# Kernel optimization log

Measured on AMD Instinct MI355X. Metric: run time of the kernel, lower is better.

## Reference

```python
import jax, jax.numpy as jnp
import numpy as np

IN_FEATURES = 4096
OUT_FEATURES = 4096
B, S = 4, 2048


def setup_inputs() -> dict:
    key = jax.random.key(0)
    k_x, k_w, k_ws, k_ss, k_b = jax.random.split(key, 5)
    x = jax.random.normal(k_x, (B, S, IN_FEATURES), dtype=jnp.float32)
    weight_quantized = jax.random.randint(k_w, (OUT_FEATURES, IN_FEATURES), -128, 128, dtype=jnp.int32).astype(jnp.int8)
    # realistic per-output-channel weight scales (small positive)
    weight_scale = jax.random.uniform(k_ws, (OUT_FEATURES,), dtype=jnp.float32, minval=1e-3, maxval=2e-2)
    # smoothing scales near 1 (clamped to [0.01, 100] in from_float)
    smooth_scale = jax.random.uniform(k_ss, (IN_FEATURES,), dtype=jnp.float32, minval=0.5, maxval=2.0)
    bias = 0.01 * jax.random.normal(k_b, (OUT_FEATURES,), dtype=jnp.float32)
    return {"x": x, "weight_quantized": weight_quantized, "weight_scale": weight_scale,
            "smooth_scale": smooth_scale, "bias": bias}


def reference(x, weight_quantized, weight_scale, smooth_scale, bias):
    # per-tensor dynamic activation quantization after smooth-scale divide
    x_smooth = x / smooth_scale                                   # [B,S,in]
    act_scale = jnp.max(jnp.abs(x_smooth)) / 127.0                # scalar
    x_quant = jnp.clip(jnp.round(x_smooth / (act_scale + 1e-5)), -128, 127).astype(jnp.int8)
    # int8 GEMM emulated in fp32 (matches torch reference: F.linear on float casts)
    out = jnp.einsum('bsi,oi->bso', x_quant.astype(jnp.float32),
                     weight_quantized.astype(jnp.float32))        # [B,S,out]
    out = out * act_scale * weight_scale                          # fused dequant
    return out + bias
```

## Files before the change

kernel.cpp:

```cpp
#include <hip/hip_runtime.h>
#include <stdint.h>

#define M_TOT 8192
#define N_TOT 4096
#define K_TOT 4096

typedef int v4i __attribute__((ext_vector_type(4)));

#define BM 256
#define BN 256
#define BK 128
#define NT (K_TOT / BK)
#define TILE_A_BYTES (BM * BK)
#define TILE_B_BYTES (BN * BK)
#define BUF_BYTES (TILE_A_BYTES + TILE_B_BYTES)

__global__ void prep_rcp(const float* __restrict__ s, float* __restrict__ r) {
  int i = blockIdx.x * blockDim.x + threadIdx.x;
  if (i < K_TOT) r[i] = 1.0f / s[i];
}

__global__ void pack_w(const int4* __restrict__ w32, int* __restrict__ w8, int n4) {
  int stride = gridDim.x * blockDim.x;
  for (int i = blockIdx.x * blockDim.x + threadIdx.x; i < n4; i += stride) {
    int4 v = w32[i];
    w8[i] = (v.x & 0xff) | ((v.y & 0xff) << 8) | ((v.z & 0xff) << 16) | (v.w << 24);
  }
}

__global__ void reduce_maxabs(const float4* __restrict__ x,
                              const float4* __restrict__ rcp4,
                              unsigned int* __restrict__ maxbits, int n4) {
  float m = 0.0f;
  int stride = gridDim.x * blockDim.x;
  for (int i = blockIdx.x * blockDim.x + threadIdx.x; i < n4; i += stride) {
    float4 v = x[i];
    float4 r = rcp4[i & (K_TOT / 4 - 1)];
    m = fmaxf(m, fabsf(v.x * r.x));
    m = fmaxf(m, fabsf(v.y * r.y));
    m = fmaxf(m, fabsf(v.z * r.z));
    m = fmaxf(m, fabsf(v.w * r.w));
  }
#pragma unroll
  for (int off = 32; off; off >>= 1) m = fmaxf(m, __shfl_xor(m, off));
  __shared__ float sm[4];
  if ((threadIdx.x & 63) == 0) sm[threadIdx.x >> 6] = m;
  __syncthreads();
  if (threadIdx.x == 0) {
    float mm = fmaxf(fmaxf(sm[0], sm[1]), fmaxf(sm[2], sm[3]));
    atomicMax(maxbits, __float_as_uint(mm));
  }
}

__global__ void quantize_x(const float4* __restrict__ x,
                           const float4* __restrict__ rcp4,
                           const unsigned int* __restrict__ maxbits,
                           int* __restrict__ xq, int n4) {
  const float d = __uint_as_float(*maxbits) / 127.0f + 1e-5f;
  const float inv = 1.0f / d;
  int stride = gridDim.x * blockDim.x;
  for (int i = blockIdx.x * blockDim.x + threadIdx.x; i < n4; i += stride) {
    float4 v = x[i];
    float4 r = rcp4[i & (K_TOT / 4 - 1)];
    int q0 = (int)fminf(fmaxf(rintf(v.x * r.x * inv), -128.0f), 127.0f);
    int q1 = (int)fminf(fmaxf(rintf(v.y * r.y * inv), -128.0f), 127.0f);
    int q2 = (int)fminf(fmaxf(rintf(v.z * r.z * inv), -128.0f), 127.0f);
    int q3 = (int)fminf(fmaxf(rintf(v.w * r.w * inv), -128.0f), 127.0f);
    xq[i] = (q0 & 0xff) | ((q1 & 0xff) << 8) | ((q2 & 0xff) << 16) | (q3 << 24);
  }
}

__global__ __launch_bounds__(512, 2) void gemm_i8(
    const int8_t* __restrict__ Aq,
    const int8_t* __restrict__ Wt,
    const unsigned int* __restrict__ maxbits,
    const float* __restrict__ wscale,
    const float* __restrict__ bias,
    float* __restrict__ out) {
  __shared__ int8_t lds[2 * BUF_BYTES];

  const int tid = threadIdx.x;
  const int lane = tid & 63;
  const int wid = tid >> 6;
  const int l16 = lane & 15;
  const int lhi = lane >> 4;
  const int m0 = blockIdx.y * BM;
  const int n0 = blockIdx.x * BN;
  const int wave_m = wid >> 2;
  const int wave_n = wid & 3;

  const int roff = lane >> 3;
  const int csel = ((lane & 7) ^ roff) << 4;
  const int8_t* Abase = Aq + (size_t)m0 * K_TOT;
  const int8_t* Bbase = Wt + (size_t)n0 * K_TOT;
  int goff[4];
#pragma unroll
  for (int c = 0; c < 4; ++c) {
    int grow = (wid * 4 + c) * 8 + roff;
    goff[c] = grow * K_TOT + csel;
  }

  auto stage = [&](int dstbuf, int koff) {
#pragma unroll
    for (int c = 0; c < 4; ++c) {
      __builtin_amdgcn_global_load_lds(
          (const __attribute__((address_space(1))) void*)(Abase + goff[c] + koff),
          (__attribute__((address_space(3))) void*)(lds + dstbuf * BUF_BYTES + (wid * 4 + c) * 1024),
          16, 0, 0);
      __builtin_amdgcn_global_load_lds(
          (const __attribute__((address_space(1))) void*)(Bbase + goff[c] + koff),
          (__attribute__((address_space(3))) void*)(lds + dstbuf * BUF_BYTES + TILE_A_BYTES + (wid * 4 + c) * 1024),
          16, 0, 0);
    }
  };

  const int sw = (l16 & 7) << 4;
  const int colA0 = (0 * 64 + lhi * 16) ^ sw;
  const int colA1 = (1 * 64 + lhi * 16) ^ sw;
  const int aRow = (wave_m * 128 + l16) * BK;
  const int bRow = (wave_n * 64 + l16) * BK;

  stage(0, 0);
  stage(1, BK);
  asm volatile("s_waitcnt vmcnt(8)" ::: "memory");
  __builtin_amdgcn_s_barrier();
  __builtin_amdgcn_sched_barrier(0);

  v4i acc[8][4] = {};

#pragma unroll 2
  for (int t = 0; t < NT; ++t) {
    const int buf = t & 1;
    const int8_t* Ab = lds + buf * BUF_BYTES;
    const int8_t* Bb = lds + buf * BUF_BYTES + TILE_A_BYTES;

    v4i a0[8], a1[8], b0[4], b1[4];
#pragma unroll
    for (int i = 0; i < 8; ++i) {
      a0[i] = *(const v4i*)(Ab + aRow + i * 2048 + colA0);
      a1[i] = *(const v4i*)(Ab + aRow + i * 2048 + colA1);
    }
#pragma unroll
    for (int j = 0; j < 4; ++j) {
      b0[j] = *(const v4i*)(Bb + bRow + j * 2048 + colA0);
      b1[j] = *(const v4i*)(Bb + bRow + j * 2048 + colA1);
    }
    asm volatile("s_waitcnt lgkmcnt(0)" ::: "memory");
    __builtin_amdgcn_sched_barrier(0);
    __builtin_amdgcn_s_barrier();
    __builtin_amdgcn_sched_barrier(0);

    const int ts = (t + 2 < NT) ? (t + 2) : (NT - 1);
    stage(buf, ts * BK);
    __builtin_amdgcn_sched_barrier(0);

    __builtin_amdgcn_s_setprio(1);
#pragma unroll
    for (int i = 0; i < 8; ++i)
#pragma unroll
      for (int j = 0; j < 4; ++j) {
        acc[i][j] = __builtin_amdgcn_mfma_i32_16x16x64_i8(a0[i], b0[j], acc[i][j], 0, 0, 0);
        acc[i][j] = __builtin_amdgcn_mfma_i32_16x16x64_i8(a1[i], b1[j], acc[i][j], 0, 0, 0);
      }
    __builtin_amdgcn_s_setprio(0);
    __builtin_amdgcn_sched_barrier(0);

    asm volatile("s_waitcnt vmcnt(8)" ::: "memory");
    __builtin_amdgcn_sched_barrier(0);
    __builtin_amdgcn_s_barrier();
    __builtin_amdgcn_sched_barrier(0);
  }

  const float ascale = __uint_as_float(*maxbits) / 127.0f;
#pragma unroll
  for (int i = 0; i < 8; ++i) {
    const int orow = m0 + wave_m * 128 + i * 16 + lhi * 4;
#pragma unroll
    for (int j = 0; j < 4; ++j) {
      const int ocol = n0 + wave_n * 64 + j * 16 + l16;
      const float wsc = wscale[ocol] * ascale;
      const float bb = bias[ocol];
#pragma unroll
      for (int r = 0; r < 4; ++r) {
        out[(size_t)(orow + r) * N_TOT + ocol] = (float)acc[i][j][r] * wsc + bb;
      }
    }
  }
}

extern "C" void kernel_launch(void* const* d_in, const int* in_sizes, int n_in,
                              void* d_out, int out_size, void* d_ws, size_t ws_size,
                              hipStream_t stream) {
  const float* x = (const float*)d_in[0];
  const int* w32 = (const int*)d_in[1];
  const float* wscale = (const float*)d_in[2];
  const float* smooth = (const float*)d_in[3];
  const float* bias = (const float*)d_in[4];
  float* out = (float*)d_out;

  unsigned int* maxbits = (unsigned int*)d_ws;
  float* rcp = (float*)((char*)d_ws + 1024);
  int8_t* xq = (int8_t*)d_ws + (1 << 20);
  int8_t* wq8 = xq + (size_t)M_TOT * K_TOT;

  hipMemsetAsync(d_ws, 0, 4, stream);

  prep_rcp<<<K_TOT / 256, 256, 0, stream>>>(smooth, rcp);

  const int nw4 = N_TOT * K_TOT / 4;
  pack_w<<<2048, 256, 0, stream>>>((const int4*)w32, (int*)wq8, nw4);

  const int n4 = M_TOT * K_TOT / 4;
  reduce_maxabs<<<2048, 256, 0, stream>>>((const float4*)x, (const float4*)rcp,
                                          maxbits, n4);
  quantize_x<<<2048, 256, 0, stream>>>((const float4*)x, (const float4*)rcp,
                                       maxbits, (int*)xq, n4);

  dim3 grid(N_TOT / BN, M_TOT / BM);
  gemm_i8<<<grid, 512, 0, stream>>>(xq, wq8, maxbits, wscale, bias, out);
}
```

Before: 232.5 us.

## Overlap LDS fragment reads with MFMAs and swizzle block order for L2 reuse

Splits the per-tile LDS fragment loads into groups and issues most of the MFMAs before the barrier and the next-stage global_load_lds. Only the last quarter of the MFMAs runs after the prefetch is issued, so LDS read latency overlaps with matrix work. It also remaps the flat block index so that consecutive workgroups are spread across M rows, which is meant to change L2 locality. The cost is more reliance on the compiler interleaving the ds_reads with the MFMAs, and less compute left to hide the global-to-LDS prefetch.

New measurement: 231.6 us. Within noise of the previous version (-0.4%).

```diff
diff --git a/kernel.cpp b/kernel.cpp
--- a/kernel.cpp
+++ b/kernel.cpp
@@ -84,8 +84,12 @@
   const int wid = tid >> 6;
   const int l16 = lane & 15;
   const int lhi = lane >> 4;
-  const int m0 = blockIdx.y * BM;
-  const int n0 = blockIdx.x * BN;
+
+  const int flat = blockIdx.y * gridDim.x + blockIdx.x;
+  const int swz = (flat & 7) * 64 + (flat >> 3);
+  const int m0 = (swz / (N_TOT / BN)) * BM;
+  const int n0 = (swz % (N_TOT / BN)) * BN;
+
   const int wave_m = wid >> 2;
   const int wave_n = wid & 3;
 
@@ -136,15 +140,36 @@
 
     v4i a0[8], a1[8], b0[4], b1[4];
 #pragma unroll
-    for (int i = 0; i < 8; ++i) {
-      a0[i] = *(const v4i*)(Ab + aRow + i * 2048 + colA0);
-      a1[i] = *(const v4i*)(Ab + aRow + i * 2048 + colA1);
-    }
-#pragma unroll
-    for (int j = 0; j < 4; ++j) {
-      b0[j] = *(const v4i*)(Bb + bRow + j * 2048 + colA0);
-      b1[j] = *(const v4i*)(Bb + bRow + j * 2048 + colA1);
-    }
+    for (int i = 0; i < 4; ++i) a0[i] = *(const v4i*)(Ab + aRow + i * 2048 + colA0);
+#pragma unroll
+    for (int j = 0; j < 4; ++j) b0[j] = *(const v4i*)(Bb + bRow + j * 2048 + colA0);
+#pragma unroll
+    for (int i = 4; i < 8; ++i) a0[i] = *(const v4i*)(Ab + aRow + i * 2048 + colA0);
+#pragma unroll
+    for (int i = 0; i < 4; ++i) a1[i] = *(const v4i*)(Ab + aRow + i * 2048 + colA1);
+#pragma unroll
+    for (int j = 0; j < 4; ++j) b1[j] = *(const v4i*)(Bb + bRow + j * 2048 + colA1);
+#pragma unroll
+    for (int i = 4; i < 8; ++i) a1[i] = *(const v4i*)(Ab + aRow + i * 2048 + colA1);
+
+    __builtin_amdgcn_s_setprio(1);
+#pragma unroll
+    for (int i = 0; i < 4; ++i)
+#pragma unroll
+      for (int j = 0; j < 4; ++j)
+        acc[i][j] = __builtin_amdgcn_mfma_i32_16x16x64_i8(a0[i], b0[j], acc[i][j], 0, 0, 0);
+#pragma unroll
+    for (int i = 4; i < 8; ++i)
+#pragma unroll
+      for (int j = 0; j < 4; ++j)
+        acc[i][j] = __builtin_amdgcn_mfma_i32_16x16x64_i8(a0[i], b0[j], acc[i][j], 0, 0, 0);
+#pragma unroll
+    for (int i = 0; i < 4; ++i)
+#pragma unroll
+      for (int j = 0; j < 4; ++j)
+        acc[i][j] = __builtin_amdgcn_mfma_i32_16x16x64_i8(a1[i], b1[j], acc[i][j], 0, 0, 0);
+    __builtin_amdgcn_s_setprio(0);
+
     asm volatile("s_waitcnt lgkmcnt(0)" ::: "memory");
     __builtin_amdgcn_sched_barrier(0);
     __builtin_amdgcn_s_barrier();
@@ -156,12 +181,10 @@
 
     __builtin_amdgcn_s_setprio(1);
 #pragma unroll
-    for (int i = 0; i < 8; ++i)
-#pragma unroll
-      for (int j = 0; j < 4; ++j) {
-        acc[i][j] = __builtin_amdgcn_mfma_i32_16x16x64_i8(a0[i], b0[j], acc[i][j], 0, 0, 0);
+    for (int i = 4; i < 8; ++i)
+#pragma unroll
+      for (int j = 0; j < 4; ++j)
         acc[i][j] = __builtin_amdgcn_mfma_i32_16x16x64_i8(a1[i], b1[j], acc[i][j], 0, 0, 0);
-      }
     __builtin_amdgcn_s_setprio(0);
     __builtin_amdgcn_sched_barrier(0);
 
```

## Deepen int8 GEMM LDS pipeline to four 64-wide K stages with block swizzle

Applied to the files above, without the earlier changes.

Restructures the GEMM main loop from two 128-wide K buffers to four 64-wide K sub-stages, keeping three stages in flight. The next global-to-LDS load is issued before the LDS reads, leaving one barrier per step instead of two. It also remaps block indices so neighbouring blocks share tiles in L2, and folds the reciprocal-of-smooth-scale kernel into the weight packing kernel to remove one launch. LDS use doubles to 128KB, which likely limits the kernel to one block per CU, and each MFMA burst per sync is half as long.

New measurement: 243.8 us. 1.05x slower.

```diff
diff --git a/kernel.cpp b/kernel.cpp
--- a/kernel.cpp
+++ b/kernel.cpp
@@ -9,18 +9,17 @@
 
 #define BM 256
 #define BN 256
-#define BK 128
-#define NT (K_TOT / BK)
-#define TILE_A_BYTES (BM * BK)
-#define TILE_B_BYTES (BN * BK)
-#define BUF_BYTES (TILE_A_BYTES + TILE_B_BYTES)
-
-__global__ void prep_rcp(const float* __restrict__ s, float* __restrict__ r) {
-  int i = blockIdx.x * blockDim.x + threadIdx.x;
-  if (i < K_TOT) r[i] = 1.0f / s[i];
-}
-
-__global__ void pack_w(const int4* __restrict__ w32, int* __restrict__ w8, int n4) {
+#define SUB 64
+#define NS (K_TOT / SUB)
+#define A_SUB (BM * SUB)
+#define B_SUB (BN * SUB)
+#define BUF_BYTES (A_SUB + B_SUB)
+
+__global__ void pack_w(const int4* __restrict__ w32, int* __restrict__ w8, int n4,
+                       const float* __restrict__ smooth, float* __restrict__ rcp) {
+  if (blockIdx.x == 0) {
+    for (int i = threadIdx.x; i < K_TOT; i += blockDim.x) rcp[i] = 1.0f / smooth[i];
+  }
   int stride = gridDim.x * blockDim.x;
   for (int i = blockIdx.x * blockDim.x + threadIdx.x; i < n4; i += stride) {
     int4 v = w32[i];
@@ -77,94 +76,85 @@
     const float* __restrict__ wscale,
     const float* __restrict__ bias,
     float* __restrict__ out) {
-  __shared__ int8_t lds[2 * BUF_BYTES];
+  __shared__ int8_t lds[4 * BUF_BYTES];
 
   const int tid = threadIdx.x;
   const int lane = tid & 63;
   const int wid = tid >> 6;
   const int l16 = lane & 15;
   const int lhi = lane >> 4;
-  const int m0 = blockIdx.y * BM;
-  const int n0 = blockIdx.x * BN;
+
+  const int flat = blockIdx.y * gridDim.x + blockIdx.x;
+  const int swz = (flat & 7) * 64 + (flat >> 3);
+  const int m0 = (swz / (N_TOT / BN)) * BM;
+  const int n0 = (swz % (N_TOT / BN)) * BN;
+
   const int wave_m = wid >> 2;
   const int wave_n = wid & 3;
 
-  const int roff = lane >> 3;
-  const int csel = ((lane & 7) ^ roff) << 4;
+  const int row_l = lane >> 2;
+  const int gcol = ((lane & 3) ^ lhi) << 4;
   const int8_t* Abase = Aq + (size_t)m0 * K_TOT;
   const int8_t* Bbase = Wt + (size_t)n0 * K_TOT;
-  int goff[4];
-#pragma unroll
-  for (int c = 0; c < 4; ++c) {
-    int grow = (wid * 4 + c) * 8 + roff;
-    goff[c] = grow * K_TOT + csel;
+  int goff[2];
+#pragma unroll
+  for (int c = 0; c < 2; ++c) {
+    int grow = (wid * 2 + c) * 16 + row_l;
+    goff[c] = grow * K_TOT + gcol;
   }
 
   auto stage = [&](int dstbuf, int koff) {
 #pragma unroll
-    for (int c = 0; c < 4; ++c) {
+    for (int c = 0; c < 2; ++c) {
       __builtin_amdgcn_global_load_lds(
           (const __attribute__((address_space(1))) void*)(Abase + goff[c] + koff),
-          (__attribute__((address_space(3))) void*)(lds + dstbuf * BUF_BYTES + (wid * 4 + c) * 1024),
+          (__attribute__((address_space(3))) void*)(lds + dstbuf * BUF_BYTES + (wid * 2 + c) * 1024),
           16, 0, 0);
       __builtin_amdgcn_global_load_lds(
           (const __attribute__((address_space(1))) void*)(Bbase + goff[c] + koff),
-          (__attribute__((address_space(3))) void*)(lds + dstbuf * BUF_BYTES + TILE_A_BYTES + (wid * 4 + c) * 1024),
+          (__attribute__((address_space(3))) void*)(lds + dstbuf * BUF_BYTES + A_SUB + (wid * 2 + c) * 1024),
           16, 0, 0);
     }
   };
 
-  const int sw = (l16 & 7) << 4;
-  const int colA0 = (0 * 64 + lhi * 16) ^ sw;
-  const int colA1 = (1 * 64 + lhi * 16) ^ sw;
-  const int aRow = (wave_m * 128 + l16) * BK;
-  const int bRow = (wave_n * 64 + l16) * BK;
+  const int slot = (lhi ^ ((l16 >> 2) & 3)) << 4;
+  const int aOff = (wave_m * 128 + l16) * SUB + slot;
+  const int bOff = (wave_n * 64 + l16) * SUB + slot;
 
   stage(0, 0);
-  stage(1, BK);
+  stage(1, SUB);
+  stage(2, 2 * SUB);
   asm volatile("s_waitcnt vmcnt(8)" ::: "memory");
   __builtin_amdgcn_s_barrier();
   __builtin_amdgcn_sched_barrier(0);
 
   v4i acc[8][4] = {};
 
-#pragma unroll 2
-  for (int t = 0; t < NT; ++t) {
-    const int buf = t & 1;
+#pragma unroll 4
+  for (int s = 0; s < NS; ++s) {
+    const int buf = s & 3;
     const int8_t* Ab = lds + buf * BUF_BYTES;
-    const int8_t* Bb = lds + buf * BUF_BYTES + TILE_A_BYTES;
-
-    v4i a0[8], a1[8], b0[4], b1[4];
-#pragma unroll
-    for (int i = 0; i < 8; ++i) {
-      a0[i] = *(const v4i*)(Ab + aRow + i * 2048 + colA0);
-      a1[i] = *(const v4i*)(Ab + aRow + i * 2048 + colA1);
-    }
-#pragma unroll
-    for (int j = 0; j < 4; ++j) {
-      b0[j] = *(const v4i*)(Bb + bRow + j * 2048 + colA0);
-      b1[j] = *(const v4i*)(Bb + bRow + j * 2048 + colA1);
-    }
-    asm volatile("s_waitcnt lgkmcnt(0)" ::: "memory");
-    __builtin_amdgcn_sched_barrier(0);
-    __builtin_amdgcn_s_barrier();
-    __builtin_amdgcn_sched_barrier(0);
-
-    const int ts = (t + 2 < NT) ? (t + 2) : (NT - 1);
-    stage(buf, ts * BK);
-    __builtin_amdgcn_sched_barrier(0);
+    const int8_t* Bb = Ab + A_SUB;
+
+    const int ts = (s + 3 < NS) ? (s + 3) : (NS - 1);
+    stage((s + 3) & 3, ts * SUB);
+
+    v4i a[8], b[4];
+#pragma unroll
+    for (int i = 0; i < 8; ++i) a[i] = *(const v4i*)(Ab + aOff + i * 1024);
+#pragma unroll
+    for (int j = 0; j < 4; ++j) b[j] = *(const v4i*)(Bb + bOff + j * 1024);
 
     __builtin_amdgcn_s_setprio(1);
 #pragma unroll
     for (int i = 0; i < 8; ++i)
 #pragma unroll
-      for (int j = 0; j < 4; ++j) {
-        acc[i][j] = __builtin_amdgcn_mfma_i32_16x16x64_i8(a0[i], b0[j], acc[i][j], 0, 0, 0);
-        acc[i][j] = __builtin_amdgcn_mfma_i32_16x16x64_i8(a1[i], b1[j], acc[i][j], 0, 0, 0);
-      }
+      for (int j = 0; j < 4; ++j)
+        acc[i][j] = __builtin_amdgcn_mfma_i32_16x16x64_i8(a[i], b[j], acc[i][j], 0, 0, 0);
     __builtin_amdgcn_s_setprio(0);
     __builtin_amdgcn_sched_barrier(0);
 
+    asm volatile("s_waitcnt lgkmcnt(0)" ::: "memory");
     asm volatile("s_waitcnt vmcnt(8)" ::: "memory");
     __builtin_amdgcn_sched_barrier(0);
     __builtin_amdgcn_s_barrier();
@@ -205,10 +195,8 @@
 
   hipMemsetAsync(d_ws, 0, 4, stream);
 
-  prep_rcp<<<K_TOT / 256, 256, 0, stream>>>(smooth, rcp);
-
   const int nw4 = N_TOT * K_TOT / 4;
-  pack_w<<<2048, 256, 0, stream>>>((const int4*)w32, (int*)wq8, nw4);
+  pack_w<<<2048, 256, 0, stream>>>((const int4*)w32, (int*)wq8, nw4, smooth, rcp);
 
   const int n4 = M_TOT * K_TOT / 4;
   reduce_maxabs<<<2048, 256, 0, stream>>>((const float4*)x, (const float4*)rcp,
```
